# Optimization experiments

Measured on AMD Instinct MI355X. Metric: run time of the kernel, lower is better.

The kernel has to match this reference:

```python
import jax, jax.numpy as jnp
import numpy as np

H = 12          # num_attention_heads
HD = 64         # head_dim
GAMMA = 0.5
LOCAL_EPS = 0.8
N_APPROX = 7


def _l1norm(x, axis):
    # torch.nn.functional.normalize(x, p=1, dim=axis)
    n = jnp.sum(jnp.abs(x), axis=axis, keepdims=True)
    return x / jnp.maximum(n, 1e-12)


def setup_inputs() -> dict:
    key = jax.random.key(0)
    ks = jax.random.split(key, 6)
    B, S, E = 2, 512, 768
    std = 1.0 / np.sqrt(E)
    hidden_states = jax.random.normal(ks[0], (B, S, E), jnp.float32)
    Wq = jax.random.normal(ks[1], (E, E), jnp.float32) * std
    Wk = jax.random.normal(ks[2], (E, E), jnp.float32) * std
    Wv = jax.random.normal(ks[3], (E, E), jnp.float32) * std
    bq = jnp.zeros((E,), jnp.float32)
    bk = jnp.zeros((E,), jnp.float32)
    bv = jnp.zeros((E,), jnp.float32)
    g = jax.random.randint(ks[4], (B * S, B * S), 0, 2, jnp.int32)
    attention_mask = jnp.zeros((B, S), jnp.float32)
    return {"hidden_states": hidden_states, "Wq": Wq, "bq": bq, "Wk": Wk,
            "bk": bk, "Wv": Wv, "bv": bv, "g": g,
            "attention_mask": attention_mask}


def reference(hidden_states, Wq, bq, Wk, bk, Wv, bv, g, attention_mask):
    B, S, E = hidden_states.shape
    BN = B * S
    x = hidden_states  # torch flattens batch-major: token index = b*S + s
    q = (x @ Wq + bq) / jnp.sqrt(jnp.float32(HD))
    k = x @ Wk + bk
    v = x @ Wv + bv
    # [B,S,E] -> [BN,H,HD] -> [H,BN,HD]
    q = q.reshape(BN, H, HD).transpose(1, 0, 2)
    k = k.reshape(BN, H, HD).transpose(1, 0, 2)
    v = v.reshape(BN, H, HD).transpose(1, 0, 2)

    # W_G[h,i,j] = exp(k_i . q_j)
    W_G = jnp.exp(jnp.einsum('hid,hjd->hij', k, q))

    # sparsification mask combined with token mask
    bool_mask = (attention_mask >= 0).reshape(-1).astype(jnp.int32)  # [BN]
    g_eff = g * (bool_mask[:, None] * bool_mask[None, :])
    W_G = jnp.where(g_eff > 0, W_G, jnp.zeros((), W_G.dtype))

    out_degree = W_G.sum(axis=2)                       # [H, BN]
    rhos = jax.lax.stop_gradient(out_degree.max(axis=1))  # [H]

    eye = jnp.eye(BN, dtype=W_G.dtype)
    Bmat = rhos[:, None, None] * eye + W_G - out_degree[:, :, None] * eye

    B_power = jnp.broadcast_to(eye, (H, BN, BN))
    L_gamma = jnp.broadcast_to(eye, (H, BN, BN))
    num = 1.0
    den = jnp.ones((H,), W_G.dtype)
    for ii in range(1, N_APPROX + 1):  # fixed 7-term power series
        num = num * (GAMMA - ii + 1) * -1.0
        den = den * (ii * rhos)
        coef = num / den                               # [H]
        B_power = jnp.einsum('hij,hjk->hik', Bmat, B_power)
        L_gamma = L_gamma + coef[:, None, None] * B_power
    L_gamma = L_gamma * (rhos[:, None, None] ** GAMMA)
    diags = jnp.diagonal(L_gamma, axis1=-2, axis2=-1)  # [H, BN]
    L_gamma = _l1norm(diags[:, :, None] * eye - L_gamma, axis=2)

    attn = (LOCAL_EPS * jnp.einsum('hij,hjd->hid', _l1norm(W_G, 2), v)
            + (1.0 - LOCAL_EPS) * jnp.einsum('hij,hjd->hid', L_gamma, v))

    # faithful to torch: raw reshape of [H,BN,HD] into [B,S,H,HD]
    out = attn.reshape(B, S, H, HD)
    out = jnp.swapaxes(out, 0, 1).reshape(S, B, E)
    return jnp.swapaxes(out, 0, 1)
```

## Files before the change

kernel.cpp:

```cpp
#include <hip/hip_runtime.h>
#include <hip/hip_bf16.h>

typedef __attribute__((ext_vector_type(4))) float f32x4;
typedef __attribute__((ext_vector_type(8))) short s16x8;

typedef const __attribute__((address_space(1))) void* gptr_t;
typedef __attribute__((address_space(3))) void* lptr_t;

__device__ __forceinline__ short f2b(float f){ __hip_bfloat16 h=__float2bfloat16(f); return *(short*)&h; }
__device__ __forceinline__ float b2f(short s){ __hip_bfloat16 h; *(short*)&h = s; return __bfloat162float(h); }

__device__ __forceinline__ void gl_lds16(const void* g, void* l){
  __builtin_amdgcn_global_load_lds((gptr_t)g, (lptr_t)l, 16, 0, 0);
}


__global__ __launch_bounds__(256) void cvt_x(const float* __restrict__ X, short* __restrict__ Xb){
  int i = blockIdx.x*256 + threadIdx.x;
  const float4* p = (const float4*)(X + (size_t)i*8);
  float4 a = p[0], b = p[1];
  s16x8 o;
  o[0]=f2b(a.x); o[1]=f2b(a.y); o[2]=f2b(a.z); o[3]=f2b(a.w);
  o[4]=f2b(b.x); o[5]=f2b(b.y); o[6]=f2b(b.z); o[7]=f2b(b.w);
  *(s16x8*)(Xb + (size_t)i*8) = o;
}

__global__ __launch_bounds__(256) void cvt_wt(const float* __restrict__ W, short* __restrict__ WT){
  __shared__ short tile[64][72];
  int bl = blockIdx.x % 12, bn = blockIdx.x / 12;
  int l0 = bl*64, n0 = bn*64;
  int t = threadIdx.x;
  #pragma unroll
  for (int p=0;p<4;p++){
    int lr = p*16 + (t>>4);
    int nc = (t&15)*4;
    float4 v = *(const float4*)(W + (size_t)(l0+lr)*768 + n0 + nc);
    tile[lr][nc+0]=f2b(v.x); tile[lr][nc+1]=f2b(v.y); tile[lr][nc+2]=f2b(v.z); tile[lr][nc+3]=f2b(v.w);
  }
  __syncthreads();
  #pragma unroll
  for (int p=0;p<2;p++){
    int nr = p*32 + (t>>3);
    int lc = (t&7)*8;
    s16x8 o;
    #pragma unroll
    for(int u=0;u<8;u++) o[u] = tile[lc+u][nr];
    *(s16x8*)(WT + (size_t)(n0+nr)*768 + l0 + lc) = o;
  }
}

__global__ __launch_bounds__(256) void vtrans(const short* __restrict__ vs, short* __restrict__ vT){
  __shared__ short tile[64][72];
  int h = blockIdx.y; int i0 = blockIdx.x*64;
  int t = threadIdx.x;
  #pragma unroll
  for(int p=0;p<2;p++){
    int ir = p*32 + (t>>3); int c8=(t&7)*8;
    *(s16x8*)&tile[ir][c8] = *(const s16x8*)(vs + (size_t)(i0+ir)*768 + h*64 + c8);
  }
  __syncthreads();
  #pragma unroll
  for(int p=0;p<2;p++){
    int dr = p*32 + (t>>3); int i8=(t&7)*8;
    s16x8 o;
    #pragma unroll
    for(int u=0;u<8;u++) o[u]=tile[i8+u][dr];
    *(s16x8*)(vT + ((size_t)h*64 + dr)*1024 + i0 + i8) = o;
  }
}

__global__ __launch_bounds__(256) void qkv_gemm(const short* __restrict__ Xb, const short* __restrict__ WT,
      const float* __restrict__ bq, const float* __restrict__ bk, const float* __restrict__ bv,
      short* __restrict__ qs, short* __restrict__ ks, short* __restrict__ vs){
  __shared__ short lA[128*32], lB[128*32];
  int mat = blockIdx.y;
  const short* B = WT + (size_t)mat*768*768;
  const float* bias = mat==0?bq:(mat==1?bk:bv);
  short* outp = mat==0?qs:(mat==1?ks:vs);
  float scale = mat==0 ? 0.125f : 1.0f;
  int tm = (blockIdx.x / 6)*128, tn = (blockIdx.x % 6)*128;
  int t=threadIdx.x, wave=t>>6, lane=t&63;
  int srow=t>>2, scol=(t&3)*8;
  int wm=(wave>>1)*64, wn=(wave&1)*64;
  f32x4 acc[4][4]={};
  for (int k0=0;k0<768;k0+=32){
    #pragma unroll
    for(int r=0;r<2;++r){
      gl_lds16(Xb + (size_t)(tm+srow+r*64)*768 + k0 + scol, lA + r*2048 + wave*512);
      gl_lds16(B  + (size_t)(tn+srow+r*64)*768 + k0 + scol, lB + r*2048 + wave*512);
    }
    __syncthreads();
    int krow=(lane>>4)*8, rl=lane&15;
    s16x8 af[4], bfr[4];
    #pragma unroll
    for(int m=0;m<4;m++) af[m] = *(s16x8*)&lA[(wm+m*16+rl)*32 + krow];
    #pragma unroll
    for(int n=0;n<4;n++) bfr[n] = *(s16x8*)&lB[(wn+n*16+rl)*32 + krow];
    #pragma unroll
    for(int m=0;m<4;m++)
      #pragma unroll
      for(int n=0;n<4;n++)
        acc[m][n]=__builtin_amdgcn_mfma_f32_16x16x32_bf16(af[m],bfr[n],acc[m][n],0,0,0);
    __syncthreads();
  }
  int r0 = tm + wm + (lane>>4)*4, c0 = tn + wn + (lane&15);
  #pragma unroll
  for(int m=0;m<4;m++)
    #pragma unroll
    for(int n=0;n<4;n++){
      int col = c0 + n*16; float bb = bias[col];
      #pragma unroll
      for(int r=0;r<4;r++){
        int row = r0 + m*16 + r;
        outp[(size_t)row*768 + col] = f2b((acc[m][n][r] + bb)*scale);
      }
    }
}

__global__ __launch_bounds__(256) void wg_gemm(const short* __restrict__ kb, const short* __restrict__ qb,
      const int* __restrict__ g, const float* __restrict__ am,
      short* __restrict__ WG, float* __restrict__ od){
  __shared__ short lK[128*64], lQ[128*64];
  int h=blockIdx.y;
  int tm=(blockIdx.x>>3)*128, tn=(blockIdx.x&7)*128;
  int t=threadIdx.x, wave=t>>6, lane=t&63;
  int srow=t>>3, scol=(t&7)*8;
  int wm=(wave>>1)*64, wn=(wave&1)*64;
  #pragma unroll
  for(int r=0;r<4;++r){
    gl_lds16(kb + (size_t)(tm+srow+r*32)*768 + h*64 + scol, lK + r*2048 + wave*512);
    gl_lds16(qb + (size_t)(tn+srow+r*32)*768 + h*64 + scol, lQ + r*2048 + wave*512);
  }
  __syncthreads();
  int rl=lane&15;
  f32x4 acc[4][4]={};
  #pragma unroll
  for(int ks=0;ks<2;ks++){
    int krow=ks*32+(lane>>4)*8;
    s16x8 af[4], bfr[4];
    #pragma unroll
    for(int m=0;m<4;m++) af[m]=*(s16x8*)&lK[(wm+m*16+rl)*64+krow];
    #pragma unroll
    for(int n=0;n<4;n++) bfr[n]=*(s16x8*)&lQ[(wn+n*16+rl)*64+krow];
    #pragma unroll
    for(int m=0;m<4;m++)
      #pragma unroll
      for(int n=0;n<4;n++)
        acc[m][n]=__builtin_amdgcn_mfma_f32_16x16x32_bf16(af[m],bfr[n],acc[m][n],0,0,0);
  }
  size_t hm=(size_t)h<<20;
  int r0=tm+wm+(lane>>4)*4, c0=tn+wn+rl;
  #pragma unroll
  for(int m=0;m<4;m++){
    float rs[4]={0.f,0.f,0.f,0.f};
    #pragma unroll
    for(int n=0;n<4;n++){
      int col=c0+n*16;
      bool mc = am[col] >= 0.0f;
      #pragma unroll
      for(int r=0;r<4;r++){
        int row=r0+m*16+r;
        float e = expf(acc[m][n][r]);
        float w = (g[(size_t)row*1024+col]>0 && am[row]>=0.0f && mc) ? e : 0.f;
        WG[hm+(size_t)row*1024+col]=f2b(w);
        rs[r]+=w;
      }
    }
    #pragma unroll
    for(int r=0;r<4;r++){
      float s=rs[r];
      #pragma unroll
      for(int off=1;off<16;off<<=1) s+=__shfl_xor(s,off);
      if(rl==0) atomicAdd(&od[(h<<10)+r0+m*16+r], s);
    }
  }
}

__global__ void rhos_k(const float* __restrict__ od, float* __restrict__ rhos){
  __shared__ float red[256];
  int h = blockIdx.x, t = threadIdx.x;
  float m = -1e30f;
  for (int i=t;i<1024;i+=256) m = fmaxf(m, od[(h<<10)+i]);
  red[t]=m; __syncthreads();
  for(int s=128;s>0;s>>=1){ if(t<s) red[t]=fmaxf(red[t],red[t+s]); __syncthreads(); }
  if(t==0) rhos[h]=red[0];
}

__global__ __launch_bounds__(256) void amat_t(const short* __restrict__ WG, const float* __restrict__ od,
      const float* __restrict__ rhos, short* __restrict__ Am, short* __restrict__ AmT,
      short* __restrict__ T){
  __shared__ short tile[64][72];
  const float b7 = -33.f/2048.f, b6 = -21.f/1024.f;
  int h = blockIdx.y; int bx = blockIdx.x;
  int rb = bx >> 4, cb = bx & 15;
  int r0 = rb*64, c0 = cb*64;
  float rho = rhos[h]; float inv = 1.0f/fmaxf(rho,1e-30f);
  size_t hm = (size_t)h<<20;
  int t = threadIdx.x;
  #pragma unroll
  for(int p=0;p<2;p++){
    int r = p*32 + (t>>3); int c8 = (t&7)*8;
    size_t base = hm + (size_t)(r0+r)*1024 + c0 + c8;
    s16x8 w = *(const s16x8*)(WG + base);
    s16x8 oa, ot;
    float dadd = (rho - od[(h<<10)+r0+r])*inv;
    #pragma unroll
    for(int u=0;u<8;u++){
      bool dg = (rb==cb) && ((c8+u)==r);
      float a = b2f(w[u])*inv + (dg ? dadd : 0.f);
      oa[u]=f2b(a);
      ot[u]=f2b(b7*a + (dg ? b6 : 0.f));
      tile[r][c8+u]=oa[u];
    }
    *(s16x8*)(Am+base)=oa; *(s16x8*)(T+base)=ot;
  }
  __syncthreads();
  #pragma unroll
  for(int p=0;p<2;p++){
    int c = p*32 + (t>>3); int r8 = (t&7)*8;
    s16x8 o;
    #pragma unroll
    for(int u=0;u<8;u++) o[u]=tile[r8+u][c];
    *(s16x8*)(AmT + hm + (size_t)(c0+c)*1024 + r0 + r8) = o;
  }
}

#define GEMM2P_PROLOG \
  __shared__ short lA[2][4096], lB[2][4096]; \
  int wg = ((int)blockIdx.x & 7)*96 + ((int)blockIdx.x >> 3); \
  int h = wg >> 6; int tile = wg & 63; \
  int tm=(tile>>3)*128, tn=(tile&7)*128; \
  size_t hm=(size_t)h<<20; \
  const short* Ag = A + hm; const short* Bg = B + hm; \
  int t=threadIdx.x, wave=t>>6, lane=t&63; \
  int srow=t>>2, scol=(t&3)*8; \
  int wm=(wave>>1)*64, wn=(wave&1)*64; \
  int krow=(lane>>4)*8, rl=lane&15; \
  f32x4 acc[4][4]={}; \
  _Pragma("unroll") \
  for(int r=0;r<2;++r){ \
    gl_lds16(Ag + (size_t)(tm+srow+r*64)*1024 + scol, &lA[0][r*2048 + wave*512]); \
    gl_lds16(Bg + (size_t)(tn+srow+r*64)*1024 + scol, &lB[0][r*2048 + wave*512]); \
  } \
  __syncthreads(); \
  int cur=0; \
  _Pragma("unroll 1") \
  for(int k0=32;k0<1024;k0+=32){ \
    _Pragma("unroll") \
    for(int r=0;r<2;++r){ \
      gl_lds16(Ag + (size_t)(tm+srow+r*64)*1024 + k0 + scol, &lA[cur^1][r*2048 + wave*512]); \
      gl_lds16(Bg + (size_t)(tn+srow+r*64)*1024 + k0 + scol, &lB[cur^1][r*2048 + wave*512]); \
    } \
    s16x8 af[4], bfr[4]; \
    _Pragma("unroll") \
    for(int m=0;m<4;m++) af[m]=*(s16x8*)&lA[cur][(wm+m*16+rl)*32+krow]; \
    _Pragma("unroll") \
    for(int n=0;n<4;n++) bfr[n]=*(s16x8*)&lB[cur][(wn+n*16+rl)*32+krow]; \
    __builtin_amdgcn_s_setprio(1); \
    _Pragma("unroll") \
    for(int m=0;m<4;m++) \
      _Pragma("unroll") \
      for(int n=0;n<4;n++) \
        acc[m][n]=__builtin_amdgcn_mfma_f32_16x16x32_bf16(af[m],bfr[n],acc[m][n],0,0,0); \
    __builtin_amdgcn_s_setprio(0); \
    __syncthreads(); \
    cur^=1; \
  } \
  { s16x8 af[4], bfr[4]; \
    _Pragma("unroll") \
    for(int m=0;m<4;m++) af[m]=*(s16x8*)&lA[cur][(wm+m*16+rl)*32+krow]; \
    _Pragma("unroll") \
    for(int n=0;n<4;n++) bfr[n]=*(s16x8*)&lB[cur][(wn+n*16+rl)*32+krow]; \
    __builtin_amdgcn_s_setprio(1); \
    _Pragma("unroll") \
    for(int m=0;m<4;m++) \
      _Pragma("unroll") \
      for(int n=0;n<4;n++) \
        acc[m][n]=__builtin_amdgcn_mfma_f32_16x16x32_bf16(af[m],bfr[n],acc[m][n],0,0,0); \
    __builtin_amdgcn_s_setprio(0); \
  } \
  int r0=tm+wm+(lane>>4)*4, c0=tn+wn+(lane&15);

__global__ __launch_bounds__(256) void gemm2p_plain(const short* __restrict__ A, const short* __restrict__ B,
      short* __restrict__ D){
  GEMM2P_PROLOG
  short* Dg = D + hm;
  #pragma unroll
  for(int m=0;m<4;m++)
    #pragma unroll
    for(int n=0;n<4;n++){
      int col=c0+n*16;
      #pragma unroll
      for(int r=0;r<4;r++)
        Dg[(size_t)(r0+m*16+r)*1024 + col]=f2b(acc[m][n][r]);
    }
}

__global__ __launch_bounds__(256) void gemm2p_epi(const short* __restrict__ A, const short* __restrict__ B,
      short* __restrict__ D, const short* __restrict__ E1, const short* __restrict__ E2,
      float c0c, float cA, float cB){
  GEMM2P_PROLOG
  short* Dg = D + hm;
  const short* E1g = E1 + hm; const short* E2g = E2 + hm;
  #pragma unroll
  for(int m=0;m<4;m++)
    #pragma unroll
    for(int n=0;n<4;n++){
      int col=c0+n*16;
      #pragma unroll
      for(int r=0;r<4;r++){
        int row=r0+m*16+r;
        size_t e = (size_t)row*1024 + col;
        float v = acc[m][n][r] + cA*b2f(E1g[e]) + cB*b2f(E2g[e]);
        if(row==col) v += c0c;
        Dg[e]=f2b(v);
      }
    }
}

__global__ __launch_bounds__(256) void gemm2p_epi_stat(const short* __restrict__ A, const short* __restrict__ B,
      short* __restrict__ D, const short* __restrict__ E1, const short* __restrict__ E2,
      float c0c, float cA, float cB, float* __restrict__ rowabs, float* __restrict__ dvp){
  GEMM2P_PROLOG
  short* Dg = D + hm;
  const short* E1g = E1 + hm; const short* E2g = E2 + hm;
  #pragma unroll
  for(int m=0;m<4;m++){
    float rs[4]={0.f,0.f,0.f,0.f};
    #pragma unroll
    for(int n=0;n<4;n++){
      int col=c0+n*16;
      #pragma unroll
      for(int r=0;r<4;r++){
        int row=r0+m*16+r;
        size_t e = (size_t)row*1024 + col;
        float v = acc[m][n][r] + cA*b2f(E1g[e]) + cB*b2f(E2g[e]);
        if(row==col){ v += c0c; dvp[(h<<10)+row] = v; }
        rs[r] += fabsf(v);
        Dg[e]=f2b(v);
      }
    }
    #pragma unroll
    for(int r=0;r<4;r++){
      float s=rs[r];
      #pragma unroll
      for(int off=1;off<16;off<<=1) s+=__shfl_xor(s,off);
      if(rl==0) atomicAdd(&rowabs[(h<<10)+r0+m*16+r], s);
    }
  }
}

__global__ __launch_bounds__(256) void attn_k(const short* __restrict__ WG, const short* __restrict__ L,
    const short* __restrict__ vT, const short* __restrict__ vs,
    const float* __restrict__ od, const float* __restrict__ dv, const float* __restrict__ rowabs,
    float* __restrict__ out){
  __shared__ short lW[128*32], lL[128*32], lV[64*32];
  int h=blockIdx.y, tm=blockIdx.x*128;
  size_t hm=(size_t)h<<20;
  int t=threadIdx.x, wave=t>>6, lane=t&63;
  int srow=t>>2, scol=(t&3)*8;
  f32x4 a1[2][4]={}, a2[2][4]={};
  for(int j0=0;j0<1024;j0+=32){
    #pragma unroll
    for(int r=0;r<2;++r){
      gl_lds16(WG + hm + (size_t)(tm+srow+r*64)*1024 + j0 + scol, lW + r*2048 + wave*512);
      gl_lds16(L  + hm + (size_t)(tm+srow+r*64)*1024 + j0 + scol, lL + r*2048 + wave*512);
    }
    gl_lds16(vT + ((size_t)h*64 + srow)*1024 + j0 + scol, lV + wave*512);
    __syncthreads();
    int krow=(lane>>4)*8, rl=lane&15;
    s16x8 fw[2], fl[2], fv[4];
    #pragma unroll
    for(int m=0;m<2;m++){
      fw[m]=*(s16x8*)&lW[(wave*32+m*16+rl)*32+krow];
      fl[m]=*(s16x8*)&lL[(wave*32+m*16+rl)*32+krow];
    }
    #pragma unroll
    for(int n=0;n<4;n++) fv[n]=*(s16x8*)&lV[(n*16+rl)*32+krow];
    #pragma unroll
    for(int m=0;m<2;m++)
      #pragma unroll
      for(int n=0;n<4;n++){
        a1[m][n]=__builtin_amdgcn_mfma_f32_16x16x32_bf16(fw[m],fv[n],a1[m][n],0,0,0);
        a2[m][n]=__builtin_amdgcn_mfma_f32_16x16x32_bf16(fl[m],fv[n],a2[m][n],0,0,0);
      }
    __syncthreads();
  }
  #pragma unroll
  for(int m=0;m<2;m++)
    #pragma unroll
    for(int r=0;r<4;r++){
      int row = tm + wave*32 + m*16 + (lane>>4)*4 + r;
      float invod = 1.0f/fmaxf(od[(h<<10)+row], 1e-12f);
      float dvi = dv[(h<<10)+row];
      float ivr = 1.0f/fmaxf(rowabs[(h<<10)+row] - fabsf(dvi), 1e-12f);
      #pragma unroll
      for(int n=0;n<4;n++){
        int d = n*16 + (lane&15);
        float vv = b2f(vs[(size_t)row*768 + h*64 + d]);
        out[(((size_t)h<<10)+row)*64 + d] = 0.8f*a1[m][n][r]*invod + 0.2f*(dvi*vv - a2[m][n][r])*ivr;
      }
    }
}

extern "C" void kernel_launch(void* const* d_in, const int* in_sizes, int n_in,
                              void* d_out, int out_size, void* d_ws, size_t ws_size,
                              hipStream_t stream){
  const float* hs = (const float*)d_in[0];
  const float* Wq = (const float*)d_in[1];
  const float* bq = (const float*)d_in[2];
  const float* Wk = (const float*)d_in[3];
  const float* bk = (const float*)d_in[4];
  const float* Wv = (const float*)d_in[5];
  const float* bv = (const float*)d_in[6];
  const int*   g  = (const int*)d_in[7];
  const float* am = (const float*)d_in[8];
  float* out = (float*)d_out;

  char* w = (char*)d_ws;
  auto alloc=[&](size_t bytes)->char*{ char* p=w; w += (bytes+255)&~(size_t)255; return p; };
  short* Xb  = (short*)alloc((size_t)1024*768*2);
  short* WT  = (short*)alloc((size_t)3*768*768*2);
  short* qs  = (short*)alloc((size_t)1024*768*2);
  short* ks  = (short*)alloc((size_t)1024*768*2);
  short* vs  = (short*)alloc((size_t)1024*768*2);
  short* vT  = (short*)alloc((size_t)12*64*1024*2);
  short* WG  = (short*)alloc((size_t)12*1024*1024*2);
  short* Am  = (short*)alloc((size_t)12*1024*1024*2);
  short* AmT = (short*)alloc((size_t)12*1024*1024*2);
  short* Tm  = (short*)alloc((size_t)12*1024*1024*2);
  short* A2  = (short*)alloc((size_t)12*1024*1024*2);
  short* A3T = (short*)alloc((size_t)12*1024*1024*2);
  float* od  = (float*)alloc((size_t)12*1024*4);
  float* rh  = (float*)alloc((size_t)64*4);
  float* dv  = (float*)alloc((size_t)12*1024*4);
  float* rab = (float*)alloc((size_t)12*1024*4);

  hipMemsetAsync(od,  0, (size_t)12*1024*4, stream);
  hipMemsetAsync(rab, 0, (size_t)12*1024*4, stream);

  cvt_x<<<384,256,0,stream>>>(hs, Xb);
  cvt_wt<<<144,256,0,stream>>>(Wq, WT);
  cvt_wt<<<144,256,0,stream>>>(Wk, WT + (size_t)768*768);
  cvt_wt<<<144,256,0,stream>>>(Wv, WT + (size_t)2*768*768);
  qkv_gemm<<<dim3(48,3),256,0,stream>>>(Xb, WT, bq,bk,bv, qs,ks,vs);
  vtrans<<<dim3(16,12),256,0,stream>>>(vs, vT);
  wg_gemm<<<dim3(64,12),256,0,stream>>>(ks, qs, g, am, WG, od);
  rhos_k<<<12,256,0,stream>>>(od, rh);
  amat_t<<<dim3(256,12),256,0,stream>>>(WG, od, rh, Am, AmT, Tm);

  const float b1=-0.5f, b2=-0.125f, b3=-1.f/16.f, b4=-5.f/128.f, b5=-7.f/256.f;
  short* V = AmT;
  short* L = Tm;
  gemm2p_plain<<<768,256,0,stream>>>(Am, AmT, A2);
  gemm2p_plain<<<768,256,0,stream>>>(AmT, A2, A3T);
  gemm2p_epi<<<768,256,0,stream>>>(Tm, A3T, V, Am, A2, b3,b4,b5);
  gemm2p_epi_stat<<<768,256,0,stream>>>(V, A3T, L, Am, A2, 1.0f,b1,b2, rab, dv);

  attn_k<<<dim3(8,12),256,0,stream>>>(WG, L, vT, vs, od, dv, rab, out);
}
```

Before: 281.4 us.

## Bit-pack sparsity mask, merge weight conversions and memsets, shrink attention tiles

The int32 sparsity mask is packed into a bitmask in a separate kernel, so the exp/mask epilogue of wg_gemm reads bits instead of a 4 MB int array (each of the 12 heads previously re-read the full mask). The three weight-conversion launches become one launch, and the two memsets become one. In the gemm2p mainloop, per-iteration address arithmetic is replaced with incrementing pointers. attn_k moves to 64-row tiles, doubling its grid from 96 to 192 blocks to fill more CUs. The packing adds a kernel launch with strided scalar reads, and __expf trades a little accuracy for speed.

Measured after the change: 280.8 us. About the same (-0.2%).

```diff
diff --git a/kernel.cpp b/kernel.cpp
--- a/kernel.cpp
+++ b/kernel.cpp
@@ -25,9 +25,13 @@
   *(s16x8*)(Xb + (size_t)i*8) = o;
 }
 
-__global__ __launch_bounds__(256) void cvt_wt(const float* __restrict__ W, short* __restrict__ WT){
+__global__ __launch_bounds__(256) void cvt_wt3(const float* __restrict__ Wq, const float* __restrict__ Wk,
+      const float* __restrict__ Wv, short* __restrict__ WT){
   __shared__ short tile[64][72];
-  int bl = blockIdx.x % 12, bn = blockIdx.x / 12;
+  int mat = blockIdx.x / 144; int bx = blockIdx.x % 144;
+  const float* W = mat==0?Wq:(mat==1?Wk:Wv);
+  short* O = WT + (size_t)mat*768*768;
+  int bl = bx % 12, bn = bx / 12;
   int l0 = bl*64, n0 = bn*64;
   int t = threadIdx.x;
   #pragma unroll
@@ -45,8 +49,17 @@
     s16x8 o;
     #pragma unroll
     for(int u=0;u<8;u++) o[u] = tile[lc+u][nr];
-    *(s16x8*)(WT + (size_t)(n0+nr)*768 + l0 + lc) = o;
-  }
+    *(s16x8*)(O + (size_t)(n0+nr)*768 + l0 + lc) = o;
+  }
+}
+
+__global__ __launch_bounds__(256) void gpack(const int* __restrict__ g, unsigned* __restrict__ gb){
+  int w = blockIdx.x*256 + threadIdx.x;
+  const int* p = g + (size_t)w*32;
+  unsigned b=0;
+  #pragma unroll
+  for(int i=0;i<32;i++) b |= (p[i]>0 ? 1u:0u) << i;
+  gb[w]=b;
 }
 
 __global__ __launch_bounds__(256) void vtrans(const short* __restrict__ vs, short* __restrict__ vT){
@@ -118,7 +131,7 @@
 }
 
 __global__ __launch_bounds__(256) void wg_gemm(const short* __restrict__ kb, const short* __restrict__ qb,
-      const int* __restrict__ g, const float* __restrict__ am,
+      const unsigned* __restrict__ gb, const float* __restrict__ am,
       short* __restrict__ WG, float* __restrict__ od){
   __shared__ short lK[128*64], lQ[128*64];
   int h=blockIdx.y;
@@ -157,11 +170,13 @@
     for(int n=0;n<4;n++){
       int col=c0+n*16;
       bool mc = am[col] >= 0.0f;
+      unsigned sh = col & 31; int wofs = col >> 5;
       #pragma unroll
       for(int r=0;r<4;r++){
         int row=r0+m*16+r;
-        float e = expf(acc[m][n][r]);
-        float w = (g[(size_t)row*1024+col]>0 && am[row]>=0.0f && mc) ? e : 0.f;
+        float e = __expf(acc[m][n][r]);
+        bool gbit = (gb[(row<<5) + wofs] >> sh) & 1u;
+        float w = (gbit && am[row]>=0.0f && mc) ? e : 0.f;
         WG[hm+(size_t)row*1024+col]=f2b(w);
         rs[r]+=w;
       }
@@ -236,21 +251,25 @@
   int srow=t>>2, scol=(t&3)*8; \
   int wm=(wave>>1)*64, wn=(wave&1)*64; \
   int krow=(lane>>4)*8, rl=lane&15; \
+  const short* pA0 = Ag + (size_t)(tm+srow)*1024 + scol; \
+  const short* pA1 = pA0 + (size_t)64*1024; \
+  const short* pB0 = Bg + (size_t)(tn+srow)*1024 + scol; \
+  const short* pB1 = pB0 + (size_t)64*1024; \
   f32x4 acc[4][4]={}; \
-  _Pragma("unroll") \
-  for(int r=0;r<2;++r){ \
-    gl_lds16(Ag + (size_t)(tm+srow+r*64)*1024 + scol, &lA[0][r*2048 + wave*512]); \
-    gl_lds16(Bg + (size_t)(tn+srow+r*64)*1024 + scol, &lB[0][r*2048 + wave*512]); \
-  } \
+  gl_lds16(pA0, &lA[0][wave*512]); \
+  gl_lds16(pA1, &lA[0][2048 + wave*512]); \
+  gl_lds16(pB0, &lB[0][wave*512]); \
+  gl_lds16(pB1, &lB[0][2048 + wave*512]); \
+  pA0+=32; pA1+=32; pB0+=32; pB1+=32; \
   __syncthreads(); \
   int cur=0; \
   _Pragma("unroll 1") \
   for(int k0=32;k0<1024;k0+=32){ \
-    _Pragma("unroll") \
-    for(int r=0;r<2;++r){ \
-      gl_lds16(Ag + (size_t)(tm+srow+r*64)*1024 + k0 + scol, &lA[cur^1][r*2048 + wave*512]); \
-      gl_lds16(Bg + (size_t)(tn+srow+r*64)*1024 + k0 + scol, &lB[cur^1][r*2048 + wave*512]); \
-    } \
+    gl_lds16(pA0, &lA[cur^1][wave*512]); \
+    gl_lds16(pA1, &lA[cur^1][2048 + wave*512]); \
+    gl_lds16(pB0, &lB[cur^1][wave*512]); \
+    gl_lds16(pB1, &lB[cur^1][2048 + wave*512]); \
+    pA0+=32; pA1+=32; pB0+=32; pB1+=32; \
     s16x8 af[4], bfr[4]; \
     _Pragma("unroll") \
     for(int m=0;m<4;m++) af[m]=*(s16x8*)&lA[cur][(wm+m*16+rl)*32+krow]; \
@@ -354,53 +373,43 @@
     const short* __restrict__ vT, const short* __restrict__ vs,
     const float* __restrict__ od, const float* __restrict__ dv, const float* __restrict__ rowabs,
     float* __restrict__ out){
-  __shared__ short lW[128*32], lL[128*32], lV[64*32];
-  int h=blockIdx.y, tm=blockIdx.x*128;
+  __shared__ short lW[64*32], lL[64*32], lV[64*32];
+  int h=blockIdx.y, tm=blockIdx.x*64;
   size_t hm=(size_t)h<<20;
   int t=threadIdx.x, wave=t>>6, lane=t&63;
   int srow=t>>2, scol=(t&3)*8;
-  f32x4 a1[2][4]={}, a2[2][4]={};
+  f32x4 a1[4]={}, a2[4]={};
   for(int j0=0;j0<1024;j0+=32){
-    #pragma unroll
-    for(int r=0;r<2;++r){
-      gl_lds16(WG + hm + (size_t)(tm+srow+r*64)*1024 + j0 + scol, lW + r*2048 + wave*512);
-      gl_lds16(L  + hm + (size_t)(tm+srow+r*64)*1024 + j0 + scol, lL + r*2048 + wave*512);
-    }
+    gl_lds16(WG + hm + (size_t)(tm+srow)*1024 + j0 + scol, lW + wave*512);
+    gl_lds16(L  + hm + (size_t)(tm+srow)*1024 + j0 + scol, lL + wave*512);
     gl_lds16(vT + ((size_t)h*64 + srow)*1024 + j0 + scol, lV + wave*512);
     __syncthreads();
     int krow=(lane>>4)*8, rl=lane&15;
-    s16x8 fw[2], fl[2], fv[4];
-    #pragma unroll
-    for(int m=0;m<2;m++){
-      fw[m]=*(s16x8*)&lW[(wave*32+m*16+rl)*32+krow];
-      fl[m]=*(s16x8*)&lL[(wave*32+m*16+rl)*32+krow];
-    }
+    s16x8 fw, fl, fv[4];
+    fw=*(s16x8*)&lW[(wave*16+rl)*32+krow];
+    fl=*(s16x8*)&lL[(wave*16+rl)*32+krow];
     #pragma unroll
     for(int n=0;n<4;n++) fv[n]=*(s16x8*)&lV[(n*16+rl)*32+krow];
     #pragma unroll
-    for(int m=0;m<2;m++)
-      #pragma unroll
-      for(int n=0;n<4;n++){
-        a1[m][n]=__builtin_amdgcn_mfma_f32_16x16x32_bf16(fw[m],fv[n],a1[m][n],0,0,0);
-        a2[m][n]=__builtin_amdgcn_mfma_f32_16x16x32_bf16(fl[m],fv[n],a2[m][n],0,0,0);
-      }
+    for(int n=0;n<4;n++){
+      a1[n]=__builtin_amdgcn_mfma_f32_16x16x32_bf16(fw,fv[n],a1[n],0,0,0);
+      a2[n]=__builtin_amdgcn_mfma_f32_16x16x32_bf16(fl,fv[n],a2[n],0,0,0);
+    }
     __syncthreads();
   }
   #pragma unroll
-  for(int m=0;m<2;m++)
-    #pragma unroll
-    for(int r=0;r<4;r++){
-      int row = tm + wave*32 + m*16 + (lane>>4)*4 + r;
-      float invod = 1.0f/fmaxf(od[(h<<10)+row], 1e-12f);
-      float dvi = dv[(h<<10)+row];
-      float ivr = 1.0f/fmaxf(rowabs[(h<<10)+row] - fabsf(dvi), 1e-12f);
-      #pragma unroll
-      for(int n=0;n<4;n++){
-        int d = n*16 + (lane&15);
-        float vv = b2f(vs[(size_t)row*768 + h*64 + d]);
-        out[(((size_t)h<<10)+row)*64 + d] = 0.8f*a1[m][n][r]*invod + 0.2f*(dvi*vv - a2[m][n][r])*ivr;
-      }
-    }
+  for(int r=0;r<4;r++){
+    int row = tm + wave*16 + (lane>>4)*4 + r;
+    float invod = 1.0f/fmaxf(od[(h<<10)+row], 1e-12f);
+    float dvi = dv[(h<<10)+row];
+    float ivr = 1.0f/fmaxf(rowabs[(h<<10)+row] - fabsf(dvi), 1e-12f);
+    #pragma unroll
+    for(int n=0;n<4;n++){
+      int d = n*16 + (lane&15);
+      float vv = b2f(vs[(size_t)row*768 + h*64 + d]);
+      out[(((size_t)h<<10)+row)*64 + d] = 0.8f*a1[n][r]*invod + 0.2f*(dvi*vv - a2[n][r])*ivr;
+    }
+  }
 }
 
 extern "C" void kernel_launch(void* const* d_in, const int* in_sizes, int n_in,
@@ -425,27 +434,26 @@
   short* ks  = (short*)alloc((size_t)1024*768*2);
   short* vs  = (short*)alloc((size_t)1024*768*2);
   short* vT  = (short*)alloc((size_t)12*64*1024*2);
+  unsigned* gb = (unsigned*)alloc((size_t)1024*32*4);
   short* WG  = (short*)alloc((size_t)12*1024*1024*2);
   short* Am  = (short*)alloc((size_t)12*1024*1024*2);
   short* AmT = (short*)alloc((size_t)12*1024*1024*2);
   short* Tm  = (short*)alloc((size_t)12*1024*1024*2);
   short* A2  = (short*)alloc((size_t)12*1024*1024*2);
   short* A3T = (short*)alloc((size_t)12*1024*1024*2);
-  float* od  = (float*)alloc((size_t)12*1024*4);
+  float* od  = (float*)alloc((size_t)2*12*1024*4);
+  float* rab = od + 12*1024;
   float* rh  = (float*)alloc((size_t)64*4);
   float* dv  = (float*)alloc((size_t)12*1024*4);
-  float* rab = (float*)alloc((size_t)12*1024*4);
-
-  hipMemsetAsync(od,  0, (size_t)12*1024*4, stream);
-  hipMemsetAsync(rab, 0, (size_t)12*1024*4, stream);
+
+  hipMemsetAsync(od, 0, (size_t)2*12*1024*4, stream);
 
   cvt_x<<<384,256,0,stream>>>(hs, Xb);
-  cvt_wt<<<144,256,0,stream>>>(Wq, WT);
-  cvt_wt<<<144,256,0,stream>>>(Wk, WT + (size_t)768*768);
-  cvt_wt<<<144,256,0,stream>>>(Wv, WT + (size_t)2*768*768);
+  cvt_wt3<<<432,256,0,stream>>>(Wq, Wk, Wv, WT);
+  gpack<<<128,256,0,stream>>>(g, gb);
   qkv_gemm<<<dim3(48,3),256,0,stream>>>(Xb, WT, bq,bk,bv, qs,ks,vs);
   vtrans<<<dim3(16,12),256,0,stream>>>(vs, vT);
-  wg_gemm<<<dim3(64,12),256,0,stream>>>(ks, qs, g, am, WG, od);
+  wg_gemm<<<dim3(64,12),256,0,stream>>>(ks, qs, gb, am, WG, od);
   rhos_k<<<12,256,0,stream>>>(od, rh);
   amat_t<<<dim3(256,12),256,0,stream>>>(WG, od, rh, Am, AmT, Tm);
 
@@ -457,5 +465,5 @@
   gemm2p_epi<<<768,256,0,stream>>>(Tm, A3T, V, Am, A2, b3,b4,b5);
   gemm2p_epi_stat<<<768,256,0,stream>>>(V, A3T, L, Am, A2, 1.0f,b1,b2, rab, dv);
 
-  attn_k<<<dim3(8,12),256,0,stream>>>(WG, L, vT, vs, od, dv, rab, out);
-}
+  attn_k<<<dim3(16,12),256,0,stream>>>(WG, L, vT, vs, od, dv, rab, out);
+}
```
